# Performance work log

Hardware: AMD Instinct MI355X
Metric: run time of the kernel (lower is better)

The kernel has to match this reference:

```python
import jax, jax.numpy as jnp
import numpy as np


def setup_inputs() -> dict:
    key = jax.random.key(0)
    k1, k2, k3 = jax.random.split(key, 3)
    N = 1_000_000
    H, W, D = 704, 704, 64  # 64m x 64m x ~6m scene at grid_factor=10 cells/m
    # points spread across the grid extent (meters)
    extent = jnp.array([64.0, 64.0, 5.0], dtype=jnp.float32)
    pc1 = jax.random.uniform(k1, (1, N, 3), dtype=jnp.float32) * extent
    flow = jax.random.normal(k2, (1, N, 3), dtype=jnp.float32) * 0.1  # ~10cm flow
    dist_grid = jax.random.uniform(k3, (H, W, D), dtype=jnp.float32) * 2.0  # precomputed DT values (meters)
    grid_min = jnp.zeros((3,), dtype=jnp.float32)  # grid origin (xmin, ymin, zmin)
    return {"pc1": pc1, "flow": flow, "dist_grid": dist_grid,
            "grid_min": grid_min, "grid_factor": 10}


def _trilinear_lookup(dist_grid, pts, grid_min, grid_factor):
    # pts: [N,3]; dist_grid: [H,W,D]. Continuous voxel index, clipped to bounds
    H, W, D = dist_grid.shape
    s = (pts - grid_min) * grid_factor  # [N,3]
    sx = jnp.clip(s[:, 0], 0.0, H - 1)
    sy = jnp.clip(s[:, 1], 0.0, W - 1)
    sz = jnp.clip(s[:, 2], 0.0, D - 1)
    x0 = jnp.floor(sx).astype(jnp.int32); x1 = jnp.minimum(x0 + 1, H - 1)
    y0 = jnp.floor(sy).astype(jnp.int32); y1 = jnp.minimum(y0 + 1, W - 1)
    z0 = jnp.floor(sz).astype(jnp.int32); z1 = jnp.minimum(z0 + 1, D - 1)
    wx = sx - x0; wy = sy - y0; wz = sz - z0
    # 8-corner gather
    c000 = dist_grid[x0, y0, z0]; c001 = dist_grid[x0, y0, z1]
    c010 = dist_grid[x0, y1, z0]; c011 = dist_grid[x0, y1, z1]
    c100 = dist_grid[x1, y0, z0]; c101 = dist_grid[x1, y0, z1]
    c110 = dist_grid[x1, y1, z0]; c111 = dist_grid[x1, y1, z1]
    c00 = c000 * (1 - wz) + c001 * wz
    c01 = c010 * (1 - wz) + c011 * wz
    c10 = c100 * (1 - wz) + c101 * wz
    c11 = c110 * (1 - wz) + c111 * wz
    c0 = c00 * (1 - wy) + c01 * wy
    c1 = c10 * (1 - wy) + c11 * wy
    return c0 * (1 - wx) + c1 * wx  # [N]


def reference(pc1, flow, dist_grid, grid_min, grid_factor):
    pts = (pc1 + flow)[0]  # squeeze batch: [N,3]
    dist = _trilinear_lookup(dist_grid, pts, grid_min, jnp.float32(grid_factor))
    return dist.mean(), dist
```

## Files before the change

### kernel.cpp

```cpp
#include <hip/hip_runtime.h>
#include <hip/hip_bf16.h>


#define GH 704
#define GW 704
#define GD 64
#define PTS 4

__global__ __launch_bounds__(256, 4) void dt_loss_kernel(
    const float* __restrict__ pc1,
    const float* __restrict__ flow,
    const float* __restrict__ grid,
    const float* __restrict__ grid_min,
    const int* __restrict__ grid_factor,
    float* __restrict__ out,
    int N)
{
    const int T = gridDim.x * blockDim.x;
    const int i0 = blockIdx.x * blockDim.x + threadIdx.x;

    const float gf = (float)(*grid_factor);
    const float gmx = grid_min[0];
    const float gmy = grid_min[1];
    const float gmz = grid_min[2];

    float px[PTS], py[PTS], pz[PTS];
    bool  act[PTS];
    #pragma unroll
    for (int j = 0; j < PTS; ++j) {
        const int i = i0 + j * T;
        act[j] = (i < N);
        const int ii = act[j] ? i : 0;
        px[j] = pc1[3 * ii + 0] + flow[3 * ii + 0];
        py[j] = pc1[3 * ii + 1] + flow[3 * ii + 1];
        pz[j] = pc1[3 * ii + 2] + flow[3 * ii + 2];
    }

    float wx[PTS], wy[PTS], wz[PTS];
    float c000[PTS], c001[PTS], c010[PTS], c011[PTS];
    float c100[PTS], c101[PTS], c110[PTS], c111[PTS];
    #pragma unroll
    for (int j = 0; j < PTS; ++j) {
        float sx = (px[j] - gmx) * gf;
        float sy = (py[j] - gmy) * gf;
        float sz = (pz[j] - gmz) * gf;
        sx = fminf(fmaxf(sx, 0.0f), (float)(GH - 1));
        sy = fminf(fmaxf(sy, 0.0f), (float)(GW - 1));
        sz = fminf(fmaxf(sz, 0.0f), (float)(GD - 1));

        const int x0 = (int)sx;
        const int y0 = (int)sy;
        const int z0 = (int)sz;
        const int x1 = min(x0 + 1, GH - 1);
        const int y1 = min(y0 + 1, GW - 1);
        const int z1 = min(z0 + 1, GD - 1);

        wx[j] = sx - (float)x0;
        wy[j] = sy - (float)y0;
        wz[j] = sz - (float)z0;

        const float* p00 = grid + ((size_t)x0 * GW + (size_t)y0) * GD;
        const float* p01 = grid + ((size_t)x0 * GW + (size_t)y1) * GD;
        const float* p10 = grid + ((size_t)x1 * GW + (size_t)y0) * GD;
        const float* p11 = grid + ((size_t)x1 * GW + (size_t)y1) * GD;

        c000[j] = p00[z0]; c001[j] = p00[z1];
        c010[j] = p01[z0]; c011[j] = p01[z1];
        c100[j] = p10[z0]; c101[j] = p10[z1];
        c110[j] = p11[z0]; c111[j] = p11[z1];
    }

    float acc = 0.0f;
    #pragma unroll
    for (int j = 0; j < PTS; ++j) {
        const float c00 = c000[j] * (1.0f - wz[j]) + c001[j] * wz[j];
        const float c01 = c010[j] * (1.0f - wz[j]) + c011[j] * wz[j];
        const float c10 = c100[j] * (1.0f - wz[j]) + c101[j] * wz[j];
        const float c11 = c110[j] * (1.0f - wz[j]) + c111[j] * wz[j];
        const float c0 = c00 * (1.0f - wy[j]) + c01 * wy[j];
        const float c1 = c10 * (1.0f - wy[j]) + c11 * wy[j];
        const float v  = c0 * (1.0f - wx[j]) + c1 * wx[j];
        if (act[j]) {
            out[1 + i0 + j * T] = v;
            acc += v;
        }
    }

    float s = acc;
    #pragma unroll
    for (int off = 32; off > 0; off >>= 1)
        s += __shfl_down(s, off, 64);

    __shared__ float wsum[4];
    const int lane = threadIdx.x & 63;
    const int wid  = threadIdx.x >> 6;
    if (lane == 0) wsum[wid] = s;
    __syncthreads();
    if (threadIdx.x == 0) {
        const float part = wsum[0] + wsum[1] + wsum[2] + wsum[3];
        atomicAdd(out, part * (1.0f / (float)N));
    }
}

extern "C" void kernel_launch(void* const* d_in, const int* in_sizes, int n_in,
                              void* d_out, int out_size, void* d_ws, size_t ws_size,
                              hipStream_t stream) {
    const float* pc1        = (const float*)d_in[0];
    const float* flow       = (const float*)d_in[1];
    const float* grid       = (const float*)d_in[2];
    const float* grid_min   = (const float*)d_in[3];
    const int*   grid_factor= (const int*)d_in[4];
    float* out = (float*)d_out;

    const int N = in_sizes[0] / 3;

    hipMemsetAsync(d_out, 0, sizeof(float), stream);

    const int block = 256;
    const int threads_needed = (N + PTS - 1) / PTS;
    const int grid_sz = (threads_needed + block - 1) / block;
    dt_loss_kernel<<<grid_sz, block, 0, stream>>>(
        pc1, flow, grid, grid_min, grid_factor, out, N);
}
```

Before: 245.9 us.

## Bin points by spatial tile before trilinear gather for cache locality

Adds a scatter pass that computes voxel coordinates and buckets points into 16x16 xy tiles using atomic counters, with an overflow list. A second kernel processes each bin, so gathers from the large distance grid hit nearby cache lines. Trilinear indexing is also simplified by clamping the base corner, which makes z neighbors adjacent. The cost is an extra kernel, atomics, workspace traffic for the float4 records, and scattered output writes.

```diff
diff --git a/kernel.cpp b/kernel.cpp
--- a/kernel.cpp
+++ b/kernel.cpp
@@ -1,12 +1,130 @@
 #include <hip/hip_runtime.h>
-#include <hip/hip_bf16.h>
 
 
 #define GH 704
 #define GW 704
 #define GD 64
+
+#define BSH   4
+#define NBX   ((GH + 15) >> 4)
+#define NBY   ((GW + 15) >> 4)
+#define NBINS (NBX * NBY)
+#define CAP   1024
+
+__device__ __forceinline__ float trilerp(const float* __restrict__ g,
+                                         float sx, float sy, float sz)
+{
+    const int x0 = min((int)sx, GH - 2);
+    const int y0 = min((int)sy, GW - 2);
+    const int z0 = min((int)sz, GD - 2);
+    const float wx = sx - (float)x0;
+    const float wy = sy - (float)y0;
+    const float wz = sz - (float)z0;
+
+    const float* p00 = g + ((size_t)x0 * GW + (size_t)y0) * GD + z0;
+    const float* p01 = p00 + GD;
+    const float* p10 = p00 + (size_t)GW * GD;
+    const float* p11 = p10 + GD;
+
+    const float c000 = p00[0], c001 = p00[1];
+    const float c010 = p01[0], c011 = p01[1];
+    const float c100 = p10[0], c101 = p10[1];
+    const float c110 = p11[0], c111 = p11[1];
+
+    const float c00 = c000 * (1.0f - wz) + c001 * wz;
+    const float c01 = c010 * (1.0f - wz) + c011 * wz;
+    const float c10 = c100 * (1.0f - wz) + c101 * wz;
+    const float c11 = c110 * (1.0f - wz) + c111 * wz;
+    const float c0  = c00 * (1.0f - wy) + c01 * wy;
+    const float c1  = c10 * (1.0f - wy) + c11 * wy;
+    return c0 * (1.0f - wx) + c1 * wx;
+}
+
+__global__ __launch_bounds__(256) void bin_scatter(
+    const float* __restrict__ pc1,
+    const float* __restrict__ flow,
+    const float* __restrict__ grid_min,
+    const int* __restrict__ grid_factor,
+    int* __restrict__ cnt,
+    int* __restrict__ ovf_cnt,
+    float4* __restrict__ slots,
+    float4* __restrict__ ovf,
+    int N)
+{
+    const int i = blockIdx.x * blockDim.x + threadIdx.x;
+    if (i >= N) return;
+
+    const float gf  = (float)(*grid_factor);
+    float sx = (pc1[3 * i + 0] + flow[3 * i + 0] - grid_min[0]) * gf;
+    float sy = (pc1[3 * i + 1] + flow[3 * i + 1] - grid_min[1]) * gf;
+    float sz = (pc1[3 * i + 2] + flow[3 * i + 2] - grid_min[2]) * gf;
+    sx = fminf(fmaxf(sx, 0.0f), (float)(GH - 1));
+    sy = fminf(fmaxf(sy, 0.0f), (float)(GW - 1));
+    sz = fminf(fmaxf(sz, 0.0f), (float)(GD - 1));
+
+    const int bin = (((int)sx) >> BSH) * NBY + (((int)sy) >> BSH);
+    const float4 rec = make_float4(sx, sy, sz, __int_as_float(i));
+
+    const int pos = atomicAdd(&cnt[bin], 1);
+    if (pos < CAP) {
+        slots[(size_t)bin * CAP + pos] = rec;
+    } else {
+        const int op = atomicAdd(ovf_cnt, 1);
+        ovf[op] = rec;
+    }
+}
+
+__global__ __launch_bounds__(256, 4) void bin_process(
+    const float* __restrict__ grid,
+    const int* __restrict__ cnt,
+    const int* __restrict__ ovf_cnt,
+    const float4* __restrict__ slots,
+    const float4* __restrict__ ovf,
+    float* __restrict__ out,
+    int N)
+{
+    float acc = 0.0f;
+
+    for (int bin = blockIdx.x; bin < NBINS; bin += gridDim.x) {
+        const int n = min(cnt[bin], CAP);
+        const float4* sl = slots + (size_t)bin * CAP;
+        for (int base = 0; base < n; base += 256) {
+            const int t = base + (int)threadIdx.x;
+            if (t < n) {
+                const float4 s = sl[t];
+                const float v = trilerp(grid, s.x, s.y, s.z);
+                out[1 + __float_as_int(s.w)] = v;
+                acc += v;
+            }
+        }
+    }
+
+    const int novf = min(*ovf_cnt, N);
+    for (int t = blockIdx.x * 256 + (int)threadIdx.x; t < novf;
+         t += gridDim.x * 256) {
+        const float4 s = ovf[t];
+        const float v = trilerp(grid, s.x, s.y, s.z);
+        out[1 + __float_as_int(s.w)] = v;
+        acc += v;
+    }
+
+    float s = acc;
+    #pragma unroll
+    for (int off = 32; off > 0; off >>= 1)
+        s += __shfl_down(s, off, 64);
+
+    __shared__ float wsum[4];
+    const int lane = threadIdx.x & 63;
+    const int wid  = threadIdx.x >> 6;
+    if (lane == 0) wsum[wid] = s;
+    __syncthreads();
+    if (threadIdx.x == 0) {
+        const float part = wsum[0] + wsum[1] + wsum[2] + wsum[3];
+        atomicAdd(out, part * (1.0f / (float)N));
+    }
+}
+
 #define PTS 4
-
 __global__ __launch_bounds__(256, 4) void dt_loss_kernel(
     const float* __restrict__ pc1,
     const float* __restrict__ flow,
@@ -24,64 +142,19 @@
     const float gmy = grid_min[1];
     const float gmz = grid_min[2];
 
-    float px[PTS], py[PTS], pz[PTS];
-    bool  act[PTS];
+    float acc = 0.0f;
     #pragma unroll
     for (int j = 0; j < PTS; ++j) {
         const int i = i0 + j * T;
-        act[j] = (i < N);
-        const int ii = act[j] ? i : 0;
-        px[j] = pc1[3 * ii + 0] + flow[3 * ii + 0];
-        py[j] = pc1[3 * ii + 1] + flow[3 * ii + 1];
-        pz[j] = pc1[3 * ii + 2] + flow[3 * ii + 2];
-    }
-
-    float wx[PTS], wy[PTS], wz[PTS];
-    float c000[PTS], c001[PTS], c010[PTS], c011[PTS];
-    float c100[PTS], c101[PTS], c110[PTS], c111[PTS];
-    #pragma unroll
-    for (int j = 0; j < PTS; ++j) {
-        float sx = (px[j] - gmx) * gf;
-        float sy = (py[j] - gmy) * gf;
-        float sz = (pz[j] - gmz) * gf;
-        sx = fminf(fmaxf(sx, 0.0f), (float)(GH - 1));
-        sy = fminf(fmaxf(sy, 0.0f), (float)(GW - 1));
-        sz = fminf(fmaxf(sz, 0.0f), (float)(GD - 1));
-
-        const int x0 = (int)sx;
-        const int y0 = (int)sy;
-        const int z0 = (int)sz;
-        const int x1 = min(x0 + 1, GH - 1);
-        const int y1 = min(y0 + 1, GW - 1);
-        const int z1 = min(z0 + 1, GD - 1);
-
-        wx[j] = sx - (float)x0;
-        wy[j] = sy - (float)y0;
-        wz[j] = sz - (float)z0;
-
-        const float* p00 = grid + ((size_t)x0 * GW + (size_t)y0) * GD;
-        const float* p01 = grid + ((size_t)x0 * GW + (size_t)y1) * GD;
-        const float* p10 = grid + ((size_t)x1 * GW + (size_t)y0) * GD;
-        const float* p11 = grid + ((size_t)x1 * GW + (size_t)y1) * GD;
-
-        c000[j] = p00[z0]; c001[j] = p00[z1];
-        c010[j] = p01[z0]; c011[j] = p01[z1];
-        c100[j] = p10[z0]; c101[j] = p10[z1];
-        c110[j] = p11[z0]; c111[j] = p11[z1];
-    }
-
-    float acc = 0.0f;
-    #pragma unroll
-    for (int j = 0; j < PTS; ++j) {
-        const float c00 = c000[j] * (1.0f - wz[j]) + c001[j] * wz[j];
-        const float c01 = c010[j] * (1.0f - wz[j]) + c011[j] * wz[j];
-        const float c10 = c100[j] * (1.0f - wz[j]) + c101[j] * wz[j];
-        const float c11 = c110[j] * (1.0f - wz[j]) + c111[j] * wz[j];
-        const float c0 = c00 * (1.0f - wy[j]) + c01 * wy[j];
-        const float c1 = c10 * (1.0f - wy[j]) + c11 * wy[j];
-        const float v  = c0 * (1.0f - wx[j]) + c1 * wx[j];
-        if (act[j]) {
-            out[1 + i0 + j * T] = v;
+        if (i < N) {
+            float sx = (pc1[3 * i + 0] + flow[3 * i + 0] - gmx) * gf;
+            float sy = (pc1[3 * i + 1] + flow[3 * i + 1] - gmy) * gf;
+            float sz = (pc1[3 * i + 2] + flow[3 * i + 2] - gmz) * gf;
+            sx = fminf(fmaxf(sx, 0.0f), (float)(GH - 1));
+            sy = fminf(fmaxf(sy, 0.0f), (float)(GW - 1));
+            sz = fminf(fmaxf(sz, 0.0f), (float)(GD - 1));
+            const float v = trilerp(grid, sx, sy, sz);
+            out[1 + i] = v;
             acc += v;
         }
     }
@@ -105,20 +178,39 @@
 extern "C" void kernel_launch(void* const* d_in, const int* in_sizes, int n_in,
                               void* d_out, int out_size, void* d_ws, size_t ws_size,
                               hipStream_t stream) {
-    const float* pc1        = (const float*)d_in[0];
-    const float* flow       = (const float*)d_in[1];
-    const float* grid       = (const float*)d_in[2];
-    const float* grid_min   = (const float*)d_in[3];
-    const int*   grid_factor= (const int*)d_in[4];
+    const float* pc1         = (const float*)d_in[0];
+    const float* flow        = (const float*)d_in[1];
+    const float* grid        = (const float*)d_in[2];
+    const float* grid_min    = (const float*)d_in[3];
+    const int*   grid_factor = (const int*)d_in[4];
     float* out = (float*)d_out;
 
     const int N = in_sizes[0] / 3;
 
+    const size_t slots_bytes = (size_t)NBINS * CAP * sizeof(float4);
+    const size_t need = 8192 + slots_bytes + (size_t)N * sizeof(float4);
+
     hipMemsetAsync(d_out, 0, sizeof(float), stream);
 
-    const int block = 256;
-    const int threads_needed = (N + PTS - 1) / PTS;
-    const int grid_sz = (threads_needed + block - 1) / block;
-    dt_loss_kernel<<<grid_sz, block, 0, stream>>>(
-        pc1, flow, grid, grid_min, grid_factor, out, N);
-}
+    if (ws_size >= need && N > 0) {
+        int*    cnt   = (int*)d_ws;
+        int*    ovfc  = (int*)((char*)d_ws + (size_t)NBINS * 4);
+        float4* slots = (float4*)((char*)d_ws + 8192);
+        float4* ovf   = (float4*)((char*)d_ws + 8192 + slots_bytes);
+
+        hipMemsetAsync(d_ws, 0, (size_t)(NBINS + 1) * 4, stream);
+
+        const int blkA = (N + 255) / 256;
+        bin_scatter<<<blkA, 256, 0, stream>>>(
+            pc1, flow, grid_min, grid_factor, cnt, ovfc, slots, ovf, N);
+
+        bin_process<<<512, 256, 0, stream>>>(
+            grid, cnt, ovfc, slots, ovf, out, N);
+    } else {
+        const int block = 256;
+        const int threads_needed = (N + PTS - 1) / PTS;
+        const int grid_sz = (threads_needed + block - 1) / block;
+        dt_loss_kernel<<<grid_sz, block, 0, stream>>>(
+            pc1, flow, grid, grid_min, grid_factor, out, N);
+    }
+}
```

Result: slower. 374.5 us (+52.3%).
